# Performance work log

Measured on AMD Instinct MI355X. Metric: run time of the kernel, lower is better.

Reference implementation:

```python
import jax, jax.numpy as jnp
import numpy as np


def phi(x):
    # ELU + 1 feature map (Katharopoulos et al. 2020)
    return jax.nn.elu(x) + 1.0


def setup_inputs() -> dict:
    key = jax.random.key(0)
    k1, k2, k3 = jax.random.split(key, 3)
    B, T, D = 2, 2048, 512
    x = jax.random.normal(k1, (B, T, D), dtype=jnp.float32)
    # torch nn.Linear stores weight as (out_features, in_features)
    w_qkv = jax.random.normal(k2, (3 * D, D), dtype=jnp.float32) * 0.02
    w_out = jax.random.normal(k3, (D, D), dtype=jnp.float32) * 0.02
    return {"x": x, "w_qkv": w_qkv, "w_out": w_out, "n_heads": 16}


def reference(x, w_qkv, w_out, n_heads):
    B, T, D = x.shape
    H = n_heads
    Dh = D // H
    qkv = x @ w_qkv.T                                   # (B,T,3D)
    qkv = qkv.reshape(B, T, 3, H, Dh).transpose(2, 0, 3, 1, 4)  # (3,B,H,T,Dh)
    q, k, v = phi(qkv[0]), phi(qkv[1]), qkv[2]
    # kv outer product: (B,H,T,Dh_k,Dh_v), causal cumsum over time
    kv = k[..., :, None] * v[..., None, :]
    kv_cumsum = jnp.cumsum(kv, axis=2)
    num = jnp.einsum('bhtd,bhtde->bhte', q, kv_cumsum)  # (B,H,T,Dh)
    k_cumsum = jnp.cumsum(k, axis=2)
    denom = jnp.einsum('bhtd,bhtd->bht', q, k_cumsum)[..., None]
    denom = jnp.maximum(denom, 1e-6)
    out = num / denom                                   # (B,H,T,Dh)
    out = out.transpose(0, 2, 1, 3).reshape(B, T, D)
    return out @ w_out.T
```

## Files before the change

### kernel.cpp

```cpp
#include <hip/hip_runtime.h>
#include <hip/hip_bf16.h>
#include <math.h>

#define B_ 2
#define T_ 2048
#define D_ 512
#define H_ 16
#define DH 32
#define L_ 64
#define C_ 32
#define NC 1024
#define VTP 72
#define CSZ 1056

typedef __attribute__((ext_vector_type(8))) short bf16x8;
typedef __attribute__((ext_vector_type(4))) float f32x4;
typedef __attribute__((ext_vector_type(4))) unsigned short u16x4;

#define AS1 __attribute__((address_space(1)))
#define AS3 __attribute__((address_space(3)))

__device__ __forceinline__ float bf2f(unsigned short u) {
    union { float f; unsigned int i; } v; v.i = ((unsigned int)u) << 16; return v.f;
}
__device__ __forceinline__ unsigned short f2bf(float f) {
    union { float f; unsigned int u; } v; v.f = f;
    unsigned int u = v.u;
    unsigned int r = u + 0x7FFFu + ((u >> 16) & 1u);
    return (unsigned short)(r >> 16);
}
__device__ __forceinline__ unsigned short f2bf_rne(float f) {
    __hip_bfloat16 h = __float2bfloat16(f);
    union { __hip_bfloat16 h; unsigned short u; } v; v.h = h; return v.u;
}
__device__ __forceinline__ float phi_s(float f) {
    return f > 0.f ? f + 1.f : __expf(f);
}
__device__ __forceinline__ bf16x8 phi_frag(bf16x8 in) {
    bf16x8 r;
    #pragma unroll
    for (int i = 0; i < 8; ++i) {
        float f = bf2f((unsigned short)in[i]);
        r[i] = (short)f2bf(phi_s(f));
    }
    return r;
}
__device__ __forceinline__ void gload_lds16(const unsigned short* g, unsigned short* l) {
    __builtin_amdgcn_global_load_lds((const AS1 unsigned int*)g, (AS3 unsigned int*)l, 16, 0, 0);
}

struct __align__(16) ShQ {
    union {
        struct { unsigned short As[2][64][32]; unsigned short Bs[2][96][32]; } g;
        struct { unsigned short Kt[DH][VTP]; unsigned short Vt[48][VTP]; } s;
    };
};

__global__ __launch_bounds__(256) void gemm_qkv_cs(const float* __restrict__ x,
                                                   const float* __restrict__ W,
                                                   unsigned short* __restrict__ qkvb,
                                                   float* __restrict__ cSf)
{
    __shared__ ShQ sh;
    const int tid = threadIdx.x;
    const int lane = tid & 63;
    const int w = tid >> 6;
    const int chunk = blockIdx.x;
    const int c = chunk & 31;
    const int h = (chunk >> 5) & 15;
    const int b = chunk >> 9;
    const size_t R0 = (size_t)(b * T_ + c * L_);

    const int sr = tid >> 3;
    const int sc = (tid & 7) * 4;
    const float* ax  = x + (R0 + sr) * 512 + sc;
    const float* wgq = W + ((size_t)(h * DH) + sr) * 512 + sc;
    const float* wgk = W + ((size_t)(D_ + h * DH) + sr) * 512 + sc;
    const float* wgv = W + ((size_t)(2 * D_ + h * DH) + sr) * 512 + sc;

    f32x4 aL[2], wL[3];
    auto load_stage = [&](int k0) {
        aL[0] = *(const f32x4*)(ax + k0);
        aL[1] = *(const f32x4*)(ax + k0 + (size_t)32 * 512);
        wL[0] = *(const f32x4*)(wgq + k0);
        wL[1] = *(const f32x4*)(wgk + k0);
        wL[2] = *(const f32x4*)(wgv + k0);
    };
    auto cvt4 = [](f32x4 v) {
        u16x4 o;
        o.x = f2bf_rne(v[0]); o.y = f2bf_rne(v[1]);
        o.z = f2bf_rne(v[2]); o.w = f2bf_rne(v[3]);
        return o;
    };
    auto write_stage = [&](int buf) {
        *(u16x4*)&sh.g.As[buf][sr][sc]      = cvt4(aL[0]);
        *(u16x4*)&sh.g.As[buf][sr + 32][sc] = cvt4(aL[1]);
        *(u16x4*)&sh.g.Bs[buf][sr][sc]      = cvt4(wL[0]);
        *(u16x4*)&sh.g.Bs[buf][sr + 32][sc] = cvt4(wL[1]);
        *(u16x4*)&sh.g.Bs[buf][sr + 64][sc] = cvt4(wL[2]);
    };

    f32x4 acc[6];
    #pragma unroll
    for (int n = 0; n < 6; ++n) acc[n] = (f32x4){0.f, 0.f, 0.f, 0.f};

    const int rr = lane & 15;
    const int fg = lane >> 4;
    const int kb = fg * 8;

    load_stage(0);
    write_stage(0);
    __syncthreads();
    int cur = 0;
    for (int k0 = 0; k0 < 512; k0 += 32) {
        const bool more = k0 + 32 < 512;
        if (more) load_stage(k0 + 32);
        bf16x8 af = *(const bf16x8*)&sh.g.As[cur][w * 16 + rr][kb];
        bf16x8 bfr[6];
        #pragma unroll
        for (int n = 0; n < 6; ++n)
            bfr[n] = *(const bf16x8*)&sh.g.Bs[cur][n * 16 + rr][kb];
        #pragma unroll
        for (int n = 0; n < 6; ++n)
            acc[n] = __builtin_amdgcn_mfma_f32_16x16x32_bf16(af, bfr[n], acc[n], 0, 0, 0);
        if (more) write_stage(cur ^ 1);
        __syncthreads();
        cur ^= 1;
    }

    {
        const int colbase[6] = { h * DH, h * DH + 16,
                                 D_ + h * DH, D_ + h * DH + 16,
                                 2 * D_ + h * DH, 2 * D_ + h * DH + 16 };
        #pragma unroll
        for (int n = 0; n < 6; ++n)
            #pragma unroll
            for (int j = 0; j < 4; ++j) {
                size_t row = R0 + w * 16 + fg * 4 + j;
                qkvb[row * 1536 + colbase[n] + rr] = f2bf(acc[n][j]);
            }
    }

    #pragma unroll
    for (int n = 2; n < 4; ++n)
        #pragma unroll
        for (int j = 0; j < 4; ++j)
            sh.s.Kt[(n - 2) * 16 + rr][w * 16 + fg * 4 + j] = f2bf(phi_s(acc[n][j]));
    #pragma unroll
    for (int n = 4; n < 6; ++n)
        #pragma unroll
        for (int j = 0; j < 4; ++j)
            sh.s.Vt[(n - 4) * 16 + rr][w * 16 + fg * 4 + j] = f2bf(acc[n][j]);
    if (rr == 0) {
        #pragma unroll
        for (int j = 0; j < 4; ++j)
            sh.s.Vt[32][w * 16 + fg * 4 + j] = 0x3F80;
    }
    __syncthreads();

    if (w < 3) {
        f32x4 a2[2];
        a2[0] = (f32x4){0.f, 0.f, 0.f, 0.f};
        a2[1] = (f32x4){0.f, 0.f, 0.f, 0.f};
        #pragma unroll
        for (int ks = 0; ks < 2; ++ks) {
            int toff = fg * 8 + ks * 32;
            bf16x8 av = *(const bf16x8*)&sh.s.Vt[w * 16 + rr][toff];
            bf16x8 bkk[2];
            #pragma unroll
            for (int n = 0; n < 2; ++n)
                bkk[n] = *(const bf16x8*)&sh.s.Kt[n * 16 + rr][toff];
            #pragma unroll
            for (int n = 0; n < 2; ++n)
                a2[n] = __builtin_amdgcn_mfma_f32_16x16x32_bf16(av, bkk[n], a2[n], 0, 0, 0);
        }
        float* outp = cSf + (size_t)chunk * CSZ;
        if (w < 2) {
            #pragma unroll
            for (int n = 0; n < 2; ++n)
                #pragma unroll
                for (int r = 0; r < 4; ++r)
                    outp[(w * 16 + fg * 4 + r) * 32 + n * 16 + rr] = a2[n][r];
        } else if (fg == 0) {
            #pragma unroll
            for (int n = 0; n < 2; ++n)
                outp[32 * 32 + n * 16 + rr] = a2[n][0];
        }
    }
}

template<int BM, bool AF32, bool OUT_BF16>
__global__ __launch_bounds__(256) void gemm_nt(const void* __restrict__ Aptr,
                                               const float* __restrict__ Wf,
                                               void* __restrict__ Cout,
                                               int N, int K)
{
    constexpr int MF = BM / 32;
    constexpr int AF4 = BM / 32;
    __shared__ unsigned short As[2][BM][32];
    __shared__ unsigned short Bs[2][128][32];
    const int tid = threadIdx.x;
    const int lane = tid & 63;
    const int wave = tid >> 6;
    const int wr = wave >> 1;
    const int wc = wave & 1;
    const size_t bm = (size_t)blockIdx.x * BM;
    const size_t bn = (size_t)blockIdx.y * 128;

    const int r8 = lane >> 3;
    const int c4 = (lane & 7) * 4;
    const int lrow = lane >> 2;
    const int lcol = (lane & 3) * 8;

    const float* agf = nullptr;
    const unsigned short* agb = nullptr;
    if constexpr (AF32) agf = (const float*)Aptr + (bm + wave * (BM / 4) + r8) * (size_t)K + c4;
    else                agb = (const unsigned short*)Aptr + (bm + wave * (BM / 4) + lrow) * (size_t)K + lcol;
    const float* wgf = Wf + (bn + wave * 32 + r8) * (size_t)K + c4;

    f32x4 aL[AF4];
    f32x4 wL[4];

    auto load_stage = [&](int buf, int k0) {
        if constexpr (AF32) {
            #pragma unroll
            for (int i = 0; i < AF4; ++i)
                aL[i] = *(const f32x4*)(agf + k0 + (size_t)(i * 8) * K);
        } else {
            gload_lds16(agb + k0, &As[buf][wave * (BM / 4)][0]);
            if constexpr (BM / 4 == 32)
                gload_lds16(agb + (size_t)16 * K + k0, &As[buf][wave * (BM / 4) + 16][0]);
        }
        #pragma unroll
        for (int i = 0; i < 4; ++i)
            wL[i] = *(const f32x4*)(wgf + k0 + (size_t)(i * 8) * K);
    };
    auto write_stage = [&](int buf) {
        if constexpr (AF32) {
            #pragma unroll
            for (int i = 0; i < AF4; ++i) {
                u16x4 o;
                o.x = f2bf_rne(aL[i][0]); o.y = f2bf_rne(aL[i][1]);
                o.z = f2bf_rne(aL[i][2]); o.w = f2bf_rne(aL[i][3]);
                *(u16x4*)&As[buf][wave * (BM / 4) + r8 + i * 8][c4] = o;
            }
        }
        #pragma unroll
        for (int i = 0; i < 4; ++i) {
            u16x4 o;
            o.x = f2bf_rne(wL[i][0]); o.y = f2bf_rne(wL[i][1]);
            o.z = f2bf_rne(wL[i][2]); o.w = f2bf_rne(wL[i][3]);
            *(u16x4*)&Bs[buf][wave * 32 + r8 + i * 8][c4] = o;
        }
    };

    f32x4 acc[MF][4];
    #pragma unroll
    for (int m = 0; m < MF; ++m)
        #pragma unroll
        for (int n = 0; n < 4; ++n)
            acc[m][n] = (f32x4){0.f, 0.f, 0.f, 0.f};

    const int rr = lane & 15;
    const int kb = (lane >> 4) * 8;

    load_stage(0, 0);
    write_stage(0);
    __syncthreads();
    int cur = 0;
    for (int k0 = 0; k0 < K; k0 += 32) {
        const bool more = k0 + 32 < K;
        if (more) load_stage(cur ^ 1, k0 + 32);
        bf16x8 af[MF], bfr[4];
        #pragma unroll
        for (int m = 0; m < MF; ++m)
            af[m] = *(const bf16x8*)&As[cur][wr * (BM / 2) + m * 16 + rr][kb];
        #pragma unroll
        for (int n = 0; n < 4; ++n)
            bfr[n] = *(const bf16x8*)&Bs[cur][wc * 64 + n * 16 + rr][kb];
        #pragma unroll
        for (int m = 0; m < MF; ++m)
            #pragma unroll
            for (int n = 0; n < 4; ++n)
                acc[m][n] = __builtin_amdgcn_mfma_f32_16x16x32_bf16(af[m], bfr[n], acc[m][n], 0, 0, 0);
        if (more) write_stage(cur ^ 1);
        __syncthreads();
        cur ^= 1;
    }

    const int cr = (lane >> 4) * 4;
    const int cc = lane & 15;
    #pragma unroll
    for (int m = 0; m < MF; ++m)
        #pragma unroll
        for (int n = 0; n < 4; ++n)
            #pragma unroll
            for (int j = 0; j < 4; ++j) {
                size_t row = bm + wr * (BM / 2) + m * 16 + cr + j;
                size_t col = bn + wc * 64 + n * 16 + cc;
                float v = acc[m][n][j];
                if (OUT_BF16) ((unsigned short*)Cout)[row * N + col] = f2bf(v);
                else          ((float*)Cout)[row * N + col] = v;
            }
}

__global__ __launch_bounds__(256) void chunk_scan(const float* __restrict__ cSf,
                                                  unsigned short* __restrict__ cSt)
{
    int idx = blockIdx.x * 256 + threadIdx.x;
    int bh = idx / CSZ;
    int r  = idx % CSZ;
    const float* src = cSf + (size_t)bh * C_ * CSZ + r;
    unsigned short* dst = cSt + (size_t)bh * C_ * CSZ + r;
    float v[C_];
    #pragma unroll
    for (int c = 0; c < C_; ++c) v[c] = src[(size_t)c * CSZ];
    float acc = 0.f;
    #pragma unroll
    for (int c = 0; c < C_; ++c) {
        dst[(size_t)c * CSZ] = f2bf(acc);
        acc += v[c];
    }
}

__global__ __launch_bounds__(256) void chunk_out(const unsigned short* __restrict__ qkv,
                                                 const unsigned short* __restrict__ cSt,
                                                 unsigned short* __restrict__ attn)
{
    __shared__ unsigned short Vt[48][VTP];
    __shared__ unsigned short Am[4][16][VTP];
    const int tid = threadIdx.x;
    const int lane = tid & 63;
    const int w = tid >> 6;
    const int chunk = blockIdx.x;
    const int c = chunk & 31;
    const int h = (chunk >> 5) & 15;
    const int b = chunk >> 9;
    const size_t rowbase = ((size_t)(b * T_ + c * L_)) * (3 * D_) + h * DH;
    const int fr = lane & 15;
    const int fg = lane >> 4;

    {
        int t = w * 16 + (lane >> 2);
        int q = lane & 3;
        const unsigned short* vp = qkv + rowbase + (size_t)t * (3 * D_) + 2 * D_ + q * 8;
        bf16x8 v0 = *(const bf16x8*)vp;
        #pragma unroll
        for (int i = 0; i < 8; ++i)
            Vt[q * 8 + i][t] = (unsigned short)v0[i];
        if (q == 0) Vt[32][t] = 0x3F80;
    }

    bf16x8 aq;
    {
        const unsigned short* qp = qkv + rowbase + (size_t)(w * 16 + fr) * (3 * D_) + fg * 8;
        aq = phi_frag(*(const bf16x8*)qp);
    }
    bf16x8 bk[4];
    #pragma unroll
    for (int n = 0; n < 4; ++n) {
        if (n <= w) {
            const unsigned short* kp = qkv + rowbase + (size_t)(n * 16 + fr) * (3 * D_) + D_ + fg * 8;
            bk[n] = phi_frag(*(const bf16x8*)kp);
        }
    }
    bf16x8 bkv[3];
    #pragma unroll
    for (int n = 0; n < 3; ++n)
        bkv[n] = *(const bf16x8*)&cSt[(size_t)chunk * CSZ + (size_t)(n * 16 + fr) * 32 + fg * 8];

    f32x4 zero = (f32x4){0.f, 0.f, 0.f, 0.f};
    f32x4 acc[3];
    #pragma unroll
    for (int n = 0; n < 3; ++n)
        acc[n] = __builtin_amdgcn_mfma_f32_16x16x32_bf16(aq, bkv[n], zero, 0, 0, 0);

    #pragma unroll
    for (int n = 0; n < 4; ++n) {
        if (n <= w) {
            f32x4 s = __builtin_amdgcn_mfma_f32_16x16x32_bf16(aq, bk[n], zero, 0, 0, 0);
            #pragma unroll
            for (int r = 0; r < 4; ++r) {
                unsigned short v = f2bf(s[r]);
                if (n == w && fr > fg * 4 + r) v = 0;
                Am[w][fg * 4 + r][n * 16 + fr] = v;
            }
        }
    }
    if ((w & 1) == 0) {
        int zc = (w + 1) * 16;
        *(uint2*)&Am[w][lane >> 2][zc + (lane & 3) * 4] = (uint2){0u, 0u};
    }
    __syncthreads();

    #pragma unroll
    for (int ks = 0; ks < 2; ++ks) {
        if (ks <= (w >> 1)) {
            bf16x8 bv[3];
            #pragma unroll
            for (int n = 0; n < 3; ++n)
                bv[n] = *(const bf16x8*)&Vt[n * 16 + fr][fg * 8 + ks * 32];
            bf16x8 aa = *(const bf16x8*)&Am[w][fr][fg * 8 + ks * 32];
            #pragma unroll
            for (int n = 0; n < 3; ++n)
                acc[n] = __builtin_amdgcn_mfma_f32_16x16x32_bf16(aa, bv[n], acc[n], 0, 0, 0);
        }
    }

    float dn[4];
    #pragma unroll
    for (int r = 0; r < 4; ++r)
        dn[r] = __shfl(acc[2][r], lane & 48);
    #pragma unroll
    for (int r = 0; r < 4; ++r) {
        float inv = 1.0f / fmaxf(dn[r], 1e-6f);
        #pragma unroll
        for (int n = 0; n < 2; ++n)
            Am[w][fg * 4 + r][n * 16 + fr] = f2bf(acc[n][r] * inv);
    }
    {
        int lrow = lane >> 2;
        int q = lane & 3;
        uint4 o = *(const uint4*)&Am[w][lrow][q * 8];
        size_t grow = (size_t)(b * T_ + c * L_ + w * 16 + lrow);
        *(uint4*)(attn + grow * D_ + h * DH + q * 8) = o;
    }
}

extern "C" void kernel_launch(void* const* d_in, const int* in_sizes, int n_in,
                              void* d_out, int out_size, void* d_ws, size_t ws_size,
                              hipStream_t stream) {
    const float* x     = (const float*)d_in[0];
    const float* w_qkv = (const float*)d_in[1];
    const float* w_out = (const float*)d_in[2];
    float* out = (float*)d_out;

    char* ws = (char*)d_ws;
    unsigned short* qkvb  = (unsigned short*)ws;
    unsigned short* attnb = (unsigned short*)(ws + 12582912);
    float* cSf            = (float*)(ws + 16777216);
    unsigned short* cSt   = (unsigned short*)(ws + 21102592);

    gemm_qkv_cs<<<NC, 256, 0, stream>>>(x, w_qkv, qkvb, cSf);

    chunk_scan<<<132, 256, 0, stream>>>(cSf, cSt);

    chunk_out<<<NC, 256, 0, stream>>>(qkvb, cSt, attnb);

    gemm_nt<64, false, false><<<dim3(4096 / 64, 512 / 128), 256, 0, stream>>>(
        attnb, w_out, out, 512, 512);
}
```

Baseline: 47.57 us.

## Precompute phi(q,k) and transposed V in QKV GEMM, drop LDS staging in chunk_out

```diff
diff --git a/kernel.cpp b/kernel.cpp
--- a/kernel.cpp
+++ b/kernel.cpp
@@ -12,6 +12,7 @@
 #define NC 1024
 #define VTP 72
 #define CSZ 1056
+#define VSZ 2112
 
 typedef __attribute__((ext_vector_type(8))) short bf16x8;
 typedef __attribute__((ext_vector_type(4))) float f32x4;
@@ -36,15 +37,6 @@
 __device__ __forceinline__ float phi_s(float f) {
     return f > 0.f ? f + 1.f : __expf(f);
 }
-__device__ __forceinline__ bf16x8 phi_frag(bf16x8 in) {
-    bf16x8 r;
-    #pragma unroll
-    for (int i = 0; i < 8; ++i) {
-        float f = bf2f((unsigned short)in[i]);
-        r[i] = (short)f2bf(phi_s(f));
-    }
-    return r;
-}
 __device__ __forceinline__ void gload_lds16(const unsigned short* g, unsigned short* l) {
     __builtin_amdgcn_global_load_lds((const AS1 unsigned int*)g, (AS3 unsigned int*)l, 16, 0, 0);
 }
@@ -59,7 +51,8 @@
 __global__ __launch_bounds__(256) void gemm_qkv_cs(const float* __restrict__ x,
                                                    const float* __restrict__ W,
                                                    unsigned short* __restrict__ qkvb,
-                                                   float* __restrict__ cSf)
+                                                   float* __restrict__ cSf,
+                                                   unsigned short* __restrict__ vTb)
 {
     __shared__ ShQ sh;
     const int tid = threadIdx.x;
@@ -137,7 +130,8 @@
             #pragma unroll
             for (int j = 0; j < 4; ++j) {
                 size_t row = R0 + w * 16 + fg * 4 + j;
-                qkvb[row * 1536 + colbase[n] + rr] = f2bf(acc[n][j]);
+                float v = (n < 4) ? phi_s(acc[n][j]) : acc[n][j];
+                qkvb[row * 1536 + colbase[n] + rr] = f2bf(v);
             }
     }
 
@@ -185,6 +179,12 @@
             #pragma unroll
             for (int n = 0; n < 2; ++n)
                 outp[32 * 32 + n * 16 + rr] = a2[n][0];
+        }
+    } else {
+        unsigned short* dst = vTb + (size_t)chunk * VSZ;
+        for (int idx = lane; idx < 264; idx += 64) {
+            int row = idx >> 3, col = (idx & 7) * 8;
+            *(bf16x8*)(dst + row * 64 + col) = *(const bf16x8*)&sh.s.Vt[row][col];
         }
     }
 }
@@ -325,9 +325,9 @@
 
 __global__ __launch_bounds__(256) void chunk_out(const unsigned short* __restrict__ qkv,
                                                  const unsigned short* __restrict__ cSt,
+                                                 const unsigned short* __restrict__ vTb,
                                                  unsigned short* __restrict__ attn)
 {
-    __shared__ unsigned short Vt[48][VTP];
     __shared__ unsigned short Am[4][16][VTP];
     const int tid = threadIdx.x;
     const int lane = tid & 63;
@@ -340,34 +340,24 @@
     const int fr = lane & 15;
     const int fg = lane >> 4;
 
-    {
-        int t = w * 16 + (lane >> 2);
-        int q = lane & 3;
-        const unsigned short* vp = qkv + rowbase + (size_t)t * (3 * D_) + 2 * D_ + q * 8;
-        bf16x8 v0 = *(const bf16x8*)vp;
-        #pragma unroll
-        for (int i = 0; i < 8; ++i)
-            Vt[q * 8 + i][t] = (unsigned short)v0[i];
-        if (q == 0) Vt[32][t] = 0x3F80;
-    }
-
-    bf16x8 aq;
-    {
-        const unsigned short* qp = qkv + rowbase + (size_t)(w * 16 + fr) * (3 * D_) + fg * 8;
-        aq = phi_frag(*(const bf16x8*)qp);
-    }
+    bf16x8 aq = *(const bf16x8*)(qkv + rowbase + (size_t)(w * 16 + fr) * (3 * D_) + fg * 8);
     bf16x8 bk[4];
     #pragma unroll
-    for (int n = 0; n < 4; ++n) {
-        if (n <= w) {
-            const unsigned short* kp = qkv + rowbase + (size_t)(n * 16 + fr) * (3 * D_) + D_ + fg * 8;
-            bk[n] = phi_frag(*(const bf16x8*)kp);
-        }
-    }
+    for (int n = 0; n < 4; ++n)
+        if (n <= w)
+            bk[n] = *(const bf16x8*)(qkv + rowbase + (size_t)(n * 16 + fr) * (3 * D_) + D_ + fg * 8);
     bf16x8 bkv[3];
     #pragma unroll
     for (int n = 0; n < 3; ++n)
         bkv[n] = *(const bf16x8*)&cSt[(size_t)chunk * CSZ + (size_t)(n * 16 + fr) * 32 + fg * 8];
+    const unsigned short* vt = vTb + (size_t)chunk * VSZ;
+    bf16x8 bv[2][3];
+    #pragma unroll
+    for (int ks = 0; ks < 2; ++ks)
+        if (ks <= (w >> 1))
+            #pragma unroll
+            for (int n = 0; n < 3; ++n)
+                bv[ks][n] = *(const bf16x8*)(vt + (size_t)(n * 16 + fr) * 64 + fg * 8 + ks * 32);
 
     f32x4 zero = (f32x4){0.f, 0.f, 0.f, 0.f};
     f32x4 acc[3];
@@ -391,19 +381,14 @@
         int zc = (w + 1) * 16;
         *(uint2*)&Am[w][lane >> 2][zc + (lane & 3) * 4] = (uint2){0u, 0u};
     }
-    __syncthreads();
 
     #pragma unroll
     for (int ks = 0; ks < 2; ++ks) {
         if (ks <= (w >> 1)) {
-            bf16x8 bv[3];
+            bf16x8 aa = *(const bf16x8*)&Am[w][fr][fg * 8 + ks * 32];
             #pragma unroll
             for (int n = 0; n < 3; ++n)
-                bv[n] = *(const bf16x8*)&Vt[n * 16 + fr][fg * 8 + ks * 32];
-            bf16x8 aa = *(const bf16x8*)&Am[w][fr][fg * 8 + ks * 32];
-            #pragma unroll
-            for (int n = 0; n < 3; ++n)
-                acc[n] = __builtin_amdgcn_mfma_f32_16x16x32_bf16(aa, bv[n], acc[n], 0, 0, 0);
+                acc[n] = __builtin_amdgcn_mfma_f32_16x16x32_bf16(aa, bv[ks][n], acc[n], 0, 0, 0);
         }
     }
 
@@ -440,12 +425,13 @@
     unsigned short* attnb = (unsigned short*)(ws + 12582912);
     float* cSf            = (float*)(ws + 16777216);
     unsigned short* cSt   = (unsigned short*)(ws + 21102592);
-
-    gemm_qkv_cs<<<NC, 256, 0, stream>>>(x, w_qkv, qkvb, cSf);
+    unsigned short* vTb   = (unsigned short*)(ws + 23265280);
+
+    gemm_qkv_cs<<<NC, 256, 0, stream>>>(x, w_qkv, qkvb, cSf, vTb);
 
     chunk_scan<<<132, 256, 0, stream>>>(cSf, cSt);
 
-    chunk_out<<<NC, 256, 0, stream>>>(qkvb, cSt, attnb);
+    chunk_out<<<NC, 256, 0, stream>>>(qkvb, cSt, vTb, attnb);
 
     gemm_nt<64, false, false><<<dim3(4096 / 64, 512 / 128), 256, 0, stream>>>(
         attnb, w_out, out, 512, 512);
```

After: 48.20 us. No clear change (+1.3%).

## Process two chunks per QKV GEMM block and store phi-applied Q/K

Applied to the files above, without the earlier changes.

```diff
diff --git a/kernel.cpp b/kernel.cpp
--- a/kernel.cpp
+++ b/kernel.cpp
@@ -36,23 +36,14 @@
 __device__ __forceinline__ float phi_s(float f) {
     return f > 0.f ? f + 1.f : __expf(f);
 }
-__device__ __forceinline__ bf16x8 phi_frag(bf16x8 in) {
-    bf16x8 r;
-    #pragma unroll
-    for (int i = 0; i < 8; ++i) {
-        float f = bf2f((unsigned short)in[i]);
-        r[i] = (short)f2bf(phi_s(f));
-    }
-    return r;
-}
 __device__ __forceinline__ void gload_lds16(const unsigned short* g, unsigned short* l) {
     __builtin_amdgcn_global_load_lds((const AS1 unsigned int*)g, (AS3 unsigned int*)l, 16, 0, 0);
 }
 
 struct __align__(16) ShQ {
     union {
-        struct { unsigned short As[2][64][32]; unsigned short Bs[2][96][32]; } g;
-        struct { unsigned short Kt[DH][VTP]; unsigned short Vt[48][VTP]; } s;
+        struct { unsigned short As[2][128][32]; unsigned short Bs[2][96][32]; } g;
+        struct { unsigned short Kt[2][DH][VTP]; unsigned short Vt[2][48][VTP]; } s;
     };
 };
 
@@ -65,11 +56,11 @@
     const int tid = threadIdx.x;
     const int lane = tid & 63;
     const int w = tid >> 6;
-    const int chunk = blockIdx.x;
-    const int c = chunk & 31;
-    const int h = (chunk >> 5) & 15;
-    const int b = chunk >> 9;
-    const size_t R0 = (size_t)(b * T_ + c * L_);
+    const int chunk0 = blockIdx.x * 2;
+    const int c0 = chunk0 & 31;
+    const int h = (chunk0 >> 5) & 15;
+    const int b = chunk0 >> 9;
+    const size_t R0 = (size_t)(b * T_ + c0 * L_);
 
     const int sr = tid >> 3;
     const int sc = (tid & 7) * 4;
@@ -78,10 +69,11 @@
     const float* wgk = W + ((size_t)(D_ + h * DH) + sr) * 512 + sc;
     const float* wgv = W + ((size_t)(2 * D_ + h * DH) + sr) * 512 + sc;
 
-    f32x4 aL[2], wL[3];
+    f32x4 aL[4], wL[3];
     auto load_stage = [&](int k0) {
-        aL[0] = *(const f32x4*)(ax + k0);
-        aL[1] = *(const f32x4*)(ax + k0 + (size_t)32 * 512);
+        #pragma unroll
+        for (int i = 0; i < 4; ++i)
+            aL[i] = *(const f32x4*)(ax + k0 + (size_t)(i * 32) * 512);
         wL[0] = *(const f32x4*)(wgq + k0);
         wL[1] = *(const f32x4*)(wgk + k0);
         wL[2] = *(const f32x4*)(wgv + k0);
@@ -93,16 +85,20 @@
         return o;
     };
     auto write_stage = [&](int buf) {
-        *(u16x4*)&sh.g.As[buf][sr][sc]      = cvt4(aL[0]);
-        *(u16x4*)&sh.g.As[buf][sr + 32][sc] = cvt4(aL[1]);
+        #pragma unroll
+        for (int i = 0; i < 4; ++i)
+            *(u16x4*)&sh.g.As[buf][sr + i * 32][sc] = cvt4(aL[i]);
         *(u16x4*)&sh.g.Bs[buf][sr][sc]      = cvt4(wL[0]);
         *(u16x4*)&sh.g.Bs[buf][sr + 32][sc] = cvt4(wL[1]);
         *(u16x4*)&sh.g.Bs[buf][sr + 64][sc] = cvt4(wL[2]);
     };
 
-    f32x4 acc[6];
-    #pragma unroll
-    for (int n = 0; n < 6; ++n) acc[n] = (f32x4){0.f, 0.f, 0.f, 0.f};
+    f32x4 acc[2][6];
+    #pragma unroll
+    for (int m = 0; m < 2; ++m)
+        #pragma unroll
+        for (int n = 0; n < 6; ++n)
+            acc[m][n] = (f32x4){0.f, 0.f, 0.f, 0.f};
 
     const int rr = lane & 15;
     const int fg = lane >> 4;
@@ -115,14 +111,18 @@
     for (int k0 = 0; k0 < 512; k0 += 32) {
         const bool more = k0 + 32 < 512;
         if (more) load_stage(k0 + 32);
-        bf16x8 af = *(const bf16x8*)&sh.g.As[cur][w * 16 + rr][kb];
-        bf16x8 bfr[6];
+        bf16x8 af[2], bfr[6];
+        #pragma unroll
+        for (int mm = 0; mm < 2; ++mm)
+            af[mm] = *(const bf16x8*)&sh.g.As[cur][w * 32 + mm * 16 + rr][kb];
         #pragma unroll
         for (int n = 0; n < 6; ++n)
             bfr[n] = *(const bf16x8*)&sh.g.Bs[cur][n * 16 + rr][kb];
         #pragma unroll
-        for (int n = 0; n < 6; ++n)
-            acc[n] = __builtin_amdgcn_mfma_f32_16x16x32_bf16(af, bfr[n], acc[n], 0, 0, 0);
+        for (int mm = 0; mm < 2; ++mm)
+            #pragma unroll
+            for (int n = 0; n < 6; ++n)
+                acc[mm][n] = __builtin_amdgcn_mfma_f32_16x16x32_bf16(af[mm], bfr[n], acc[mm][n], 0, 0, 0);
         if (more) write_stage(cur ^ 1);
         __syncthreads();
         cur ^= 1;
@@ -133,58 +133,68 @@
                                  D_ + h * DH, D_ + h * DH + 16,
                                  2 * D_ + h * DH, 2 * D_ + h * DH + 16 };
         #pragma unroll
-        for (int n = 0; n < 6; ++n)
+        for (int mm = 0; mm < 2; ++mm)
+            #pragma unroll
+            for (int n = 0; n < 6; ++n)
+                #pragma unroll
+                for (int j = 0; j < 4; ++j) {
+                    size_t row = R0 + w * 32 + mm * 16 + fg * 4 + j;
+                    float v = (n < 4) ? phi_s(acc[mm][n][j]) : acc[mm][n][j];
+                    qkvb[row * 1536 + colbase[n] + rr] = f2bf(v);
+                }
+    }
+
+    {
+        const int ci = w >> 1;
+        const int wl = w & 1;
+        #pragma unroll
+        for (int mm = 0; mm < 2; ++mm)
             #pragma unroll
             for (int j = 0; j < 4; ++j) {
-                size_t row = R0 + w * 16 + fg * 4 + j;
-                qkvb[row * 1536 + colbase[n] + rr] = f2bf(acc[n][j]);
+                int t = wl * 32 + mm * 16 + fg * 4 + j;
+                sh.s.Kt[ci][rr][t]      = f2bf(phi_s(acc[mm][2][j]));
+                sh.s.Kt[ci][16 + rr][t] = f2bf(phi_s(acc[mm][3][j]));
+                sh.s.Vt[ci][rr][t]      = f2bf(acc[mm][4][j]);
+                sh.s.Vt[ci][16 + rr][t] = f2bf(acc[mm][5][j]);
+                if (rr == 0) sh.s.Vt[ci][32][t] = 0x3F80;
             }
     }
-
-    #pragma unroll
-    for (int n = 2; n < 4; ++n)
-        #pragma unroll
-        for (int j = 0; j < 4; ++j)
-            sh.s.Kt[(n - 2) * 16 + rr][w * 16 + fg * 4 + j] = f2bf(phi_s(acc[n][j]));
-    #pragma unroll
-    for (int n = 4; n < 6; ++n)
-        #pragma unroll
-        for (int j = 0; j < 4; ++j)
-            sh.s.Vt[(n - 4) * 16 + rr][w * 16 + fg * 4 + j] = f2bf(acc[n][j]);
-    if (rr == 0) {
-        #pragma unroll
-        for (int j = 0; j < 4; ++j)
-            sh.s.Vt[32][w * 16 + fg * 4 + j] = 0x3F80;
-    }
     __syncthreads();
 
-    if (w < 3) {
-        f32x4 a2[2];
-        a2[0] = (f32x4){0.f, 0.f, 0.f, 0.f};
-        a2[1] = (f32x4){0.f, 0.f, 0.f, 0.f};
-        #pragma unroll
-        for (int ks = 0; ks < 2; ++ks) {
-            int toff = fg * 8 + ks * 32;
-            bf16x8 av = *(const bf16x8*)&sh.s.Vt[w * 16 + rr][toff];
-            bf16x8 bkk[2];
-            #pragma unroll
-            for (int n = 0; n < 2; ++n)
-                bkk[n] = *(const bf16x8*)&sh.s.Kt[n * 16 + rr][toff];
-            #pragma unroll
-            for (int n = 0; n < 2; ++n)
-                a2[n] = __builtin_amdgcn_mfma_f32_16x16x32_bf16(av, bkk[n], a2[n], 0, 0, 0);
-        }
+    {
+        const int ci = w >> 1;
+        const int chunk = chunk0 + ci;
         float* outp = cSf + (size_t)chunk * CSZ;
-        if (w < 2) {
-            #pragma unroll
-            for (int n = 0; n < 2; ++n)
+        const int nm = (w & 1) ? 1 : 2;
+        #pragma unroll
+        for (int mi = 0; mi < 2; ++mi) {
+            if (mi < nm) {
+                int m = (w & 1) ? 1 : mi * 2;
+                f32x4 a2[2];
+                a2[0] = (f32x4){0.f, 0.f, 0.f, 0.f};
+                a2[1] = (f32x4){0.f, 0.f, 0.f, 0.f};
                 #pragma unroll
-                for (int r = 0; r < 4; ++r)
-                    outp[(w * 16 + fg * 4 + r) * 32 + n * 16 + rr] = a2[n][r];
-        } else if (fg == 0) {
-            #pragma unroll
-            for (int n = 0; n < 2; ++n)
-                outp[32 * 32 + n * 16 + rr] = a2[n][0];
+                for (int ks = 0; ks < 2; ++ks) {
+                    int toff = fg * 8 + ks * 32;
+                    bf16x8 av = *(const bf16x8*)&sh.s.Vt[ci][m * 16 + rr][toff];
+                    #pragma unroll
+                    for (int n = 0; n < 2; ++n) {
+                        bf16x8 bkk = *(const bf16x8*)&sh.s.Kt[ci][n * 16 + rr][toff];
+                        a2[n] = __builtin_amdgcn_mfma_f32_16x16x32_bf16(av, bkk, a2[n], 0, 0, 0);
+                    }
+                }
+                if (m < 2) {
+                    #pragma unroll
+                    for (int n = 0; n < 2; ++n)
+                        #pragma unroll
+                        for (int r = 0; r < 4; ++r)
+                            outp[(m * 16 + fg * 4 + r) * 32 + n * 16 + rr] = a2[n][r];
+                } else if (fg == 0) {
+                    #pragma unroll
+                    for (int n = 0; n < 2; ++n)
+                        outp[32 * 32 + n * 16 + rr] = a2[n][0];
+                }
+            }
         }
     }
 }
@@ -351,19 +361,12 @@
         if (q == 0) Vt[32][t] = 0x3F80;
     }
 
-    bf16x8 aq;
-    {
-        const unsigned short* qp = qkv + rowbase + (size_t)(w * 16 + fr) * (3 * D_) + fg * 8;
-        aq = phi_frag(*(const bf16x8*)qp);
-    }
+    bf16x8 aq = *(const bf16x8*)(qkv + rowbase + (size_t)(w * 16 + fr) * (3 * D_) + fg * 8);
     bf16x8 bk[4];
     #pragma unroll
-    for (int n = 0; n < 4; ++n) {
-        if (n <= w) {
-            const unsigned short* kp = qkv + rowbase + (size_t)(n * 16 + fr) * (3 * D_) + D_ + fg * 8;
-            bk[n] = phi_frag(*(const bf16x8*)kp);
-        }
-    }
+    for (int n = 0; n < 4; ++n)
+        if (n <= w)
+            bk[n] = *(const bf16x8*)(qkv + rowbase + (size_t)(n * 16 + fr) * (3 * D_) + D_ + fg * 8);
     bf16x8 bkv[3];
     #pragma unroll
     for (int n = 0; n < 3; ++n)
@@ -441,7 +444,7 @@
     float* cSf            = (float*)(ws + 16777216);
     unsigned short* cSt   = (unsigned short*)(ws + 21102592);
 
-    gemm_qkv_cs<<<NC, 256, 0, stream>>>(x, w_qkv, qkvb, cSf);
+    gemm_qkv_cs<<<NC / 2, 256, 0, stream>>>(x, w_qkv, qkvb, cSf);
 
     chunk_scan<<<132, 256, 0, stream>>>(cSf, cSt);
 
```

New measurement: 52.23 us. 9.8% more time.
